# Kernel optimization log

Measured on AMD Instinct MI355X. Metric: run time of the kernel, lower is better.

The kernel has to match this reference:

```python
import jax, jax.numpy as jnp
import numpy as np

IMAGE_SIZE = 1024
PATCH_SIZE = 16
GRID = IMAGE_SIZE // PATCH_SIZE  # 64


def _downsample_nearest(mask, p):
    # torch F.interpolate(mode='nearest') with integer downscale p picks input index i*p
    b = mask.shape[0]
    return mask[:, 0, ::p, ::p].reshape(b, -1)  # (b, N)


def setup_inputs() -> dict:
    key = jax.random.key(0)
    k1, k2, k3, k4 = jax.random.split(key, 4)
    b, N, c = 8, GRID * GRID, 256
    ep_mask_embed = jax.random.normal(k1, (b, N, c), dtype=jnp.float32)
    query_mask_embed = jax.random.normal(k2, (b, N, c), dtype=jnp.float32)
    ep_mask = jax.random.randint(k3, (b, 1, IMAGE_SIZE, IMAGE_SIZE), 0, 2).astype(jnp.float32)
    query_mask = jax.random.randint(k4, (b, 1, IMAGE_SIZE, IMAGE_SIZE), 0, 2).astype(jnp.float32)
    return {"ep_mask_embed": ep_mask_embed, "ep_mask": ep_mask,
            "query_mask_embed": query_mask_embed, "query_mask": query_mask}


def reference(ep_mask_embed, ep_mask, query_mask_embed, query_mask):
    b, N, c = ep_mask_embed.shape
    ep_m = _downsample_nearest(ep_mask, PATCH_SIZE)      # (b, N)
    q_m = _downsample_nearest(query_mask, PATCH_SIZE)    # (b, N)

    # masked episode centers
    pos_center = jnp.einsum('bnc,bn->bc', ep_mask_embed, ep_m) / (jnp.sum(ep_m, -1, keepdims=True) + 0.1)
    rev = 1.0 - ep_m
    neg_center = jnp.einsum('bnc,bn->bc', ep_mask_embed, rev) / (jnp.sum(rev, -1, keepdims=True) + 0.1)

    # per-token squared distance to the corresponding center, summed over channels
    sq_pos = jnp.sum((query_mask_embed - pos_center[:, None, :]) ** 2, axis=-1)  # (b, N)
    sq_neg = jnp.sum((query_mask_embed - neg_center[:, None, :]) ** 2, axis=-1)  # (b, N)

    n_pos = jnp.sum(q_m, axis=-1)            # (b,)
    n_neg = jnp.sum(1.0 - q_m, axis=-1)      # (b,)

    pos_loss = jnp.where(n_pos > 0,
                         jnp.sum(sq_pos * q_m, -1) / (jnp.maximum(n_pos, 1.0) * c),
                         0.0)
    neg_loss = jnp.where(n_neg > 0,
                         jnp.sum(sq_neg * (1.0 - q_m), -1) / (jnp.maximum(n_neg, 1.0) * c),
                         0.0)
    center_loss = pos_loss + neg_loss
    return jnp.stack([jnp.mean(center_loss), jnp.mean(pos_loss), jnp.mean(neg_loss)])
```

## Files before the change

### kernel.cpp

```cpp
#include <hip/hip_runtime.h>

#define BATCH 8
#define NTOK 4096
#define CH 256
#define IMG 1024
#define PATCH 16
#define CHUNKS 32
#define TPB (NTOK / CHUNKS)
#define PART_STRIDE 520
#define NBLK_STATS (2 * BATCH * CHUNKS)


__device__ __forceinline__ float wave_reduce_sum(float v) {
    for (int off = 32; off > 0; off >>= 1) v += __shfl_down(v, off, 64);
    return v;
}

__global__ __launch_bounds__(256) void stats_kernel(
    const float* __restrict__ ep_e, const float* __restrict__ ep_m,
    const float* __restrict__ q_e,  const float* __restrict__ q_m,
    float* __restrict__ ws, float* __restrict__ out)
{
    const int bid = blockIdx.x;
    const int tid = threadIdx.x;
    if (bid == 0 && tid < 3) out[tid] = 0.f;

    const bool is_q = (bid >= BATCH * CHUNKS);
    const int lb    = bid & (BATCH * CHUNKS - 1);
    const int b     = lb >> 5;
    const int start = (lb & (CHUNKS - 1)) * TPB;

    const float* __restrict__ embed = is_q ? q_e : ep_e;
    const float* __restrict__ mask  = is_q ? q_m : ep_m;

    const int w = tid >> 6, lane = tid & 63, cbase = lane << 2;

    float4 accW = {0.f, 0.f, 0.f, 0.f};
    float4 accS = {0.f, 0.f, 0.f, 0.f};
    float accA = 0.f, accB = 0.f, accm = 0.f;

    const float* ebase = embed + (size_t)(b * NTOK + start) * CH + cbase;
    const size_t mrow  = (size_t)b * IMG * IMG + (size_t)((start >> 6) * PATCH) * IMG;

    const int t0 = w * 32;
    #pragma unroll
    for (int bat = 0; bat < 4; ++bat) {
        float4 e[8];
        float  mm[8];
        #pragma unroll
        for (int k = 0; k < 8; ++k) {
            const int t = t0 + bat * 8 + k;
            mm[k] = mask[mrow + (size_t)((t >> 6) * PATCH) * IMG + (size_t)((t & 63) * PATCH)];
            e[k]  = *reinterpret_cast<const float4*>(ebase + (size_t)t * CH);
        }
        #pragma unroll
        for (int k = 0; k < 8; ++k) {
            const float m = mm[k];
            accW.x += m * e[k].x; accW.y += m * e[k].y;
            accW.z += m * e[k].z; accW.w += m * e[k].w;
            accS.x += e[k].x;     accS.y += e[k].y;
            accS.z += e[k].z;     accS.w += e[k].w;
            if (is_q) {
                const float d = e[k].x * e[k].x + e[k].y * e[k].y
                              + e[k].z * e[k].z + e[k].w * e[k].w;
                accA += m * d;
                accB += d;
            }
            accm += m;
        }
    }

    __shared__ __align__(16) float ldsW[4][CH];
    __shared__ __align__(16) float ldsS[4][CH];
    __shared__ float ldsA[4], ldsB[4], ldsM[4];

    *reinterpret_cast<float4*>(&ldsW[w][cbase]) = accW;
    *reinterpret_cast<float4*>(&ldsS[w][cbase]) = accS;
    if (is_q) {
        accA = wave_reduce_sum(accA);
        accB = wave_reduce_sum(accB);
    }
    if (lane == 0) { ldsA[w] = accA; ldsB[w] = accB; ldsM[w] = accm; }
    __syncthreads();

    float* p = ws + (size_t)bid * PART_STRIDE;
    const int c = tid;
    p[c]      = ldsW[0][c] + ldsW[1][c] + ldsW[2][c] + ldsW[3][c];
    p[CH + c] = ldsS[0][c] + ldsS[1][c] + ldsS[2][c] + ldsS[3][c];
    if (tid == 0) {
        p[512] = ldsM[0] + ldsM[1] + ldsM[2] + ldsM[3];
        p[513] = is_q ? (ldsA[0] + ldsA[1] + ldsA[2] + ldsA[3]) : 0.f;
        p[514] = is_q ? (ldsB[0] + ldsB[1] + ldsB[2] + ldsB[3]) : 0.f;
    }
}

__global__ __launch_bounds__(256) void finalize_kernel(
    const float* __restrict__ ws, float* __restrict__ out)
{
    const int b   = blockIdx.x;
    const int tid = threadIdx.x;

    float pn = 0.f, se = 0.f, uu = 0.f, vv = 0.f;
    #pragma unroll 8
    for (int k = 0; k < CHUNKS; ++k) {
        const float* pe = ws + (size_t)(b * CHUNKS + k) * PART_STRIDE;
        const float* pq = pe + (size_t)(BATCH * CHUNKS) * PART_STRIDE;
        pn += pe[tid];      se += pe[CH + tid];
        uu += pq[tid];      vv += pq[CH + tid];
    }

    __shared__ float sc[4];
    if (tid < 64) {
        float c0 = 0.f, a0 = 0.f, b0 = 0.f, n0 = 0.f;
        if (tid < CHUNKS) {
            const float* pe = ws + (size_t)(b * CHUNKS + tid) * PART_STRIDE;
            const float* pq = pe + (size_t)(BATCH * CHUNKS) * PART_STRIDE;
            c0 = pe[512]; a0 = pq[513]; b0 = pq[514]; n0 = pq[512];
        }
        c0 = wave_reduce_sum(c0); a0 = wave_reduce_sum(a0);
        b0 = wave_reduce_sum(b0); n0 = wave_reduce_sum(n0);
        if (tid == 0) { sc[0] = c0; sc[1] = a0; sc[2] = b0; sc[3] = n0; }
    }
    __syncthreads();

    const float cnt = sc[0], A = sc[1], Bv = sc[2], np = sc[3];
    const float pc = pn / (cnt + 0.1f);
    const float nc = (se - pn) / (((float)NTOK - cnt) + 0.1f);

    float4 t;
    t.x = uu * pc;
    t.y = (vv - uu) * nc;
    t.z = pc * pc;
    t.w = nc * nc;

    __shared__ float4 red[256];
    red[tid] = t;
    __syncthreads();
    for (int s = 128; s > 0; s >>= 1) {
        if (tid < s) {
            red[tid].x += red[tid + s].x;
            red[tid].y += red[tid + s].y;
            red[tid].z += red[tid + s].z;
            red[tid].w += red[tid + s].w;
        }
        __syncthreads();
    }

    if (tid == 0) {
        const float nn = (float)NTOK - np;
        const float pos_term = A - 2.f * red[0].x + np * red[0].z;
        const float neg_term = (Bv - A) - 2.f * red[0].y + nn * red[0].w;
        const float pos_loss = (np > 0.f) ? pos_term / (fmaxf(np, 1.f) * (float)CH) : 0.f;
        const float neg_loss = (nn > 0.f) ? neg_term / (fmaxf(nn, 1.f) * (float)CH) : 0.f;
        const float inv_b = 1.f / (float)BATCH;
        atomicAdd(&out[0], (pos_loss + neg_loss) * inv_b);
        atomicAdd(&out[1], pos_loss * inv_b);
        atomicAdd(&out[2], neg_loss * inv_b);
    }
}

extern "C" void kernel_launch(void* const* d_in, const int* in_sizes, int n_in,
                              void* d_out, int out_size, void* d_ws, size_t ws_size,
                              hipStream_t stream) {
    const float* ep_e = (const float*)d_in[0];
    const float* ep_m = (const float*)d_in[1];
    const float* q_e  = (const float*)d_in[2];
    const float* q_m  = (const float*)d_in[3];
    float* out = (float*)d_out;
    float* ws  = (float*)d_ws;

    stats_kernel<<<NBLK_STATS, 256, 0, stream>>>(ep_e, ep_m, q_e, q_m, ws, out);
    finalize_kernel<<<BATCH, 256, 0, stream>>>(ws, out);
}
```

Measured before the change: 22.86 us.

## Fuse stats and finalize into one kernel via last-block atomic counters

```diff
diff --git a/kernel.cpp b/kernel.cpp
--- a/kernel.cpp
+++ b/kernel.cpp
@@ -5,10 +5,12 @@
 #define CH 256
 #define IMG 1024
 #define PATCH 16
-#define CHUNKS 32
+#define CHUNKS 64
 #define TPB (NTOK / CHUNKS)
 #define PART_STRIDE 520
 #define NBLK_STATS (2 * BATCH * CHUNKS)
+#define SB (NBLK_STATS * PART_STRIDE)
+#define ARRIVALS_PER_BATCH (2 * CHUNKS)
 
 
 __device__ __forceinline__ float wave_reduce_sum(float v) {
@@ -16,19 +18,19 @@
     return v;
 }
 
-__global__ __launch_bounds__(256) void stats_kernel(
+__global__ __launch_bounds__(256) void fused_kernel(
     const float* __restrict__ ep_e, const float* __restrict__ ep_m,
     const float* __restrict__ q_e,  const float* __restrict__ q_m,
     float* __restrict__ ws, float* __restrict__ out)
 {
     const int bid = blockIdx.x;
     const int tid = threadIdx.x;
-    if (bid == 0 && tid < 3) out[tid] = 0.f;
 
     const bool is_q = (bid >= BATCH * CHUNKS);
     const int lb    = bid & (BATCH * CHUNKS - 1);
-    const int b     = lb >> 5;
-    const int start = (lb & (CHUNKS - 1)) * TPB;
+    const int b     = lb >> 6;
+    const int chunk = lb & (CHUNKS - 1);
+    const int start = chunk * TPB;
 
     const float* __restrict__ embed = is_q ? q_e : ep_e;
     const float* __restrict__ mask  = is_q ? q_m : ep_m;
@@ -40,17 +42,17 @@
     float accA = 0.f, accB = 0.f, accm = 0.f;
 
     const float* ebase = embed + (size_t)(b * NTOK + start) * CH + cbase;
-    const size_t mrow  = (size_t)b * IMG * IMG + (size_t)((start >> 6) * PATCH) * IMG;
+    const float* mrow = mask + (size_t)b * IMG * IMG + (size_t)(chunk * PATCH) * IMG;
 
-    const int t0 = w * 32;
+    const int t0 = w * 16;
     #pragma unroll
-    for (int bat = 0; bat < 4; ++bat) {
+    for (int bat = 0; bat < 2; ++bat) {
         float4 e[8];
         float  mm[8];
         #pragma unroll
         for (int k = 0; k < 8; ++k) {
             const int t = t0 + bat * 8 + k;
-            mm[k] = mask[mrow + (size_t)((t >> 6) * PATCH) * IMG + (size_t)((t & 63) * PATCH)];
+            mm[k] = mrow[(size_t)t * PATCH];
             e[k]  = *reinterpret_cast<const float4*>(ebase + (size_t)t * CH);
         }
         #pragma unroll
@@ -92,31 +94,35 @@
         p[513] = is_q ? (ldsA[0] + ldsA[1] + ldsA[2] + ldsA[3]) : 0.f;
         p[514] = is_q ? (ldsB[0] + ldsB[1] + ldsB[2] + ldsB[3]) : 0.f;
     }
-}
 
-__global__ __launch_bounds__(256) void finalize_kernel(
-    const float* __restrict__ ws, float* __restrict__ out)
-{
-    const int b   = blockIdx.x;
-    const int tid = threadIdx.x;
+    unsigned int* cnt1 = (unsigned int*)(ws + SB + 16);
+    unsigned int* cnt2 = (unsigned int*)(ws + SB + 24);
+    __shared__ unsigned s_last;
+    __syncthreads();
+    if (tid == 0) {
+        __threadfence();
+        unsigned old = atomicAdd(&cnt1[b], 1u);
+        s_last = (old == ARRIVALS_PER_BATCH - 1u);
+    }
+    __syncthreads();
+    if (!s_last) return;
+
+    __threadfence();
 
     float pn = 0.f, se = 0.f, uu = 0.f, vv = 0.f;
     #pragma unroll 8
     for (int k = 0; k < CHUNKS; ++k) {
         const float* pe = ws + (size_t)(b * CHUNKS + k) * PART_STRIDE;
         const float* pq = pe + (size_t)(BATCH * CHUNKS) * PART_STRIDE;
-        pn += pe[tid];      se += pe[CH + tid];
-        uu += pq[tid];      vv += pq[CH + tid];
+        pn += pe[c];      se += pe[CH + c];
+        uu += pq[c];      vv += pq[CH + c];
     }
 
     __shared__ float sc[4];
     if (tid < 64) {
-        float c0 = 0.f, a0 = 0.f, b0 = 0.f, n0 = 0.f;
-        if (tid < CHUNKS) {
-            const float* pe = ws + (size_t)(b * CHUNKS + tid) * PART_STRIDE;
-            const float* pq = pe + (size_t)(BATCH * CHUNKS) * PART_STRIDE;
-            c0 = pe[512]; a0 = pq[513]; b0 = pq[514]; n0 = pq[512];
-        }
+        const float* pe = ws + (size_t)(b * CHUNKS + tid) * PART_STRIDE;
+        const float* pq = pe + (size_t)(BATCH * CHUNKS) * PART_STRIDE;
+        float c0 = pe[512], a0 = pq[513], b0 = pq[514], n0 = pq[512];
         c0 = wave_reduce_sum(c0); a0 = wave_reduce_sum(a0);
         b0 = wave_reduce_sum(b0); n0 = wave_reduce_sum(n0);
         if (tid == 0) { sc[0] = c0; sc[1] = a0; sc[2] = b0; sc[3] = n0; }
@@ -152,10 +158,23 @@
         const float neg_term = (Bv - A) - 2.f * red[0].y + nn * red[0].w;
         const float pos_loss = (np > 0.f) ? pos_term / (fmaxf(np, 1.f) * (float)CH) : 0.f;
         const float neg_loss = (nn > 0.f) ? neg_term / (fmaxf(nn, 1.f) * (float)CH) : 0.f;
-        const float inv_b = 1.f / (float)BATCH;
-        atomicAdd(&out[0], (pos_loss + neg_loss) * inv_b);
-        atomicAdd(&out[1], pos_loss * inv_b);
-        atomicAdd(&out[2], neg_loss * inv_b);
+        ws[SB + b]     = pos_loss;
+        ws[SB + 8 + b] = neg_loss;
+        __threadfence();
+        unsigned old2 = atomicAdd(cnt2, 1u);
+        if (old2 == BATCH - 1u) {
+            __threadfence();
+            float sp = 0.f, sn = 0.f;
+            #pragma unroll
+            for (int bb = 0; bb < BATCH; ++bb) {
+                sp += ws[SB + bb];
+                sn += ws[SB + 8 + bb];
+            }
+            const float inv_b = 1.f / (float)BATCH;
+            out[0] = (sp + sn) * inv_b;
+            out[1] = sp * inv_b;
+            out[2] = sn * inv_b;
+        }
     }
 }
 
@@ -169,6 +188,7 @@
     float* out = (float*)d_out;
     float* ws  = (float*)d_ws;
 
-    stats_kernel<<<NBLK_STATS, 256, 0, stream>>>(ep_e, ep_m, q_e, q_m, ws, out);
-    finalize_kernel<<<BATCH, 256, 0, stream>>>(ws, out);
+    hipMemsetAsync((char*)ws + (size_t)(SB + 16) * sizeof(float), 0,
+                   9 * sizeof(unsigned int), stream);
+    fused_kernel<<<NBLK_STATS, 256, 0, stream>>>(ep_e, ep_m, q_e, q_m, ws, out);
 }
```

New measurement: 67.49 us. +195.2%, slower.
